# Optimization experiments

Hardware: AMD Instinct MI355X
Metric: run time of the kernel (lower is better)

## Reference

```python
import math
import jax, jax.numpy as jnp
import numpy as np

WS = 4            # window size
LS = 2 * WS       # local context size
NH = 8            # num heads
DIM = 128
EPS = 1e-5


def setup_inputs() -> dict:
    key = jax.random.key(0)
    ks = jax.random.split(key, 8)
    B, C, H, W = 4, DIM, 48, 48
    features = jax.random.normal(ks[0], (B, C, H, W), dtype=jnp.float32)
    s = 0.02
    return {
        'features': features,
        'ln_w': jnp.ones((C,), jnp.float32),
        'ln_b': jnp.zeros((C,), jnp.float32),
        'q_w': jax.random.normal(ks[1], (C, C), jnp.float32) * s,
        'q_b': jnp.zeros((C,), jnp.float32),
        'kv_w': jax.random.normal(ks[2], (2 * C, C), jnp.float32) * s,
        'kv_b': jnp.zeros((2 * C,), jnp.float32),
        'out_w': jax.random.normal(ks[3], (C, C), jnp.float32) * s,
        'out_b': jnp.zeros((C,), jnp.float32),
    }


def _avgpool_tokens(x, k):
    # x: [B,C,H,W] -> [B, (H//k)*(W//k), C]
    B, C, H, W = x.shape
    t = x.reshape(B, C, H // k, k, W // k, k).mean(axis=(3, 5))
    return t.reshape(B, C, -1).transpose(0, 2, 1)


def reference(features, ln_w, ln_b, q_w, q_b, kv_w, kv_b, out_w, out_b):
    B, C, H, W = features.shape
    Hw, Ww = H // WS, W // WS
    nw = Hw * Ww
    hd = C // NH

    # ---- window partition: [B,C,H,W] -> [B*nw, WS*WS, C]
    qt = features.reshape(B, C, Hw, WS, Ww, WS).transpose(0, 2, 4, 3, 5, 1)
    qt = qt.reshape(B * nw, WS * WS, C)

    # ---- LayerNorm(dim)
    mu = qt.mean(-1, keepdims=True)
    var = qt.var(-1, keepdims=True)
    qt = (qt - mu) / jnp.sqrt(var + EPS) * ln_w + ln_b

    # ---- local context: pad to target, unfold kernel=LS stride=WS
    target = (int(math.sqrt(nw)) - 1) * WS + LS
    ph, pw = max(0, target - H), max(0, target - W)
    pad = ((0, 0), (0, 0), (ph // 2, ph - ph // 2), (pw // 2, pw - pw // 2))
    padded = jnp.pad(features, pad)
    # channel order of patches is (C, kh, kw), same as torch unfold
    patches = jax.lax.conv_general_dilated_patches(
        padded, filter_shape=(LS, LS), window_strides=(WS, WS), padding='VALID')
    local = patches.reshape(B, C, LS * LS, nw).transpose(0, 3, 2, 1)
    local = local.reshape(B * nw, LS * LS, C)

    # ---- multi-scale pooled tokens, broadcast to each window
    mid = _avgpool_tokens(features, 2)      # [B, M, C]
    glo = _avgpool_tokens(features, 4)      # [B, G, C]
    mid = jnp.broadcast_to(mid[:, None], (B, nw) + mid.shape[1:]).reshape(B * nw, -1, C)
    glo = jnp.broadcast_to(glo[:, None], (B, nw) + glo.shape[1:]).reshape(B * nw, -1, C)

    kv_tokens = jnp.concatenate([local, mid, glo], axis=1)  # [B*nw, Nkv, C]

    # ---- projections (torch Linear: x @ W.T + b)
    queries = qt @ q_w.T + q_b
    kv = kv_tokens @ kv_w.T + kv_b
    keys, values = kv[..., :C], kv[..., C:]

    # ---- multi-head attention
    Nq, Nkv = queries.shape[1], keys.shape[1]
    q = queries.reshape(-1, Nq, NH, hd)
    k = keys.reshape(-1, Nkv, NH, hd)
    v = values.reshape(-1, Nkv, NH, hd)
    scores = jnp.einsum('bqhd,bkhd->bhqk', q, k) / math.sqrt(hd)
    weights = jax.nn.softmax(scores, axis=-1)
    attended = jnp.einsum('bhqk,bkhd->bqhd', weights, v).reshape(-1, Nq, C)

    out = attended @ out_w.T + out_b

    # ---- window reconstruction -> [B,C,H,W]
    out = out.reshape(B, Hw, Ww, WS, WS, C).transpose(0, 5, 1, 3, 2, 4)
    out = out.reshape(B, C, H, W)
    return out + features
```

## Files before the change

kernel.cpp:

```cpp
#include <hip/hip_runtime.h>


typedef unsigned short u16;
typedef short v8s __attribute__((ext_vector_type(8)));
typedef v8s __attribute__((may_alias)) v8s_am;
typedef short v4s __attribute__((ext_vector_type(4)));
typedef v4s __attribute__((may_alias)) v4s_am;
typedef float v4f __attribute__((ext_vector_type(4)));

#define MFMA_BF16(a, b, c) __builtin_amdgcn_mfma_f32_16x16x32_bf16(a, b, c, 0, 0, 0)

#if __has_builtin(__builtin_amdgcn_mfma_f32_16x16x16bf16_1k)
#define MFMA16(a, b, c) __builtin_amdgcn_mfma_f32_16x16x16bf16_1k(a, b, c, 0, 0, 0)
#else
static __device__ __forceinline__ v4f mfma16_fb(v4s a, v4s b, v4f c) {
    v8s a8 = {a[0], a[1], a[2], a[3], 0, 0, 0, 0};
    v8s b8 = {b[0], b[1], b[2], b[3], 0, 0, 0, 0};
    return MFMA_BF16(a8, b8, c);
}
#define MFMA16(a, b, c) mfma16_fb(a, b, c)
#endif

#if __has_builtin(__builtin_amdgcn_exp2f)
#define EXP2(x) __builtin_amdgcn_exp2f(x)
#else
#define EXP2(x) exp2f(x)
#endif

__device__ __forceinline__ float b2f(u16 u) {
    union { unsigned int i; float f; } x;
    x.i = ((unsigned int)u) << 16;
    return x.f;
}
__device__ __forceinline__ u16 f2b(float f) {
    union { float f; unsigned int i; } x;
    x.f = f;
    unsigned int u = x.i;
    return (u16)((u + 0x7fffu + ((u >> 16) & 1u)) >> 16);
}

__global__ __launch_bounds__(256) void k_prep_gemm(
    const float* __restrict__ F,
    const float* __restrict__ qw, const float* __restrict__ kvw,
    const float* __restrict__ ow,
    const float* __restrict__ lnw, const float* __restrict__ lnb,
    const float* __restrict__ kvb,
    u16* __restrict__ Xt, u16* __restrict__ Wb, float* __restrict__ MuRs,
    u16* __restrict__ KVg, u16* __restrict__ VTg)
{
    __shared__ u16 SH[17408];
    int blk = blockIdx.x;
    int t = threadIdx.x;

    if (blk >= 304) {
        u16 (*Al)[136] = (u16(*)[136])SH;
        u16 (*Wl)[136] = (u16(*)[136])(SH + 8704);
        int gb = blk - 304;
        int tm = (gb % 45) * 64, tn = (gb / 45) * 64;
        {
            int seg = t & 15, r0 = t >> 4;
#pragma unroll
            for (int i = 0; i < 4; ++i) {
                int r = r0 + 16 * i;
                const float* src = kvw + (size_t)(tn + r) * 128 + seg * 8;
                float4 v0 = *(const float4*)src;
                float4 v1 = *(const float4*)(src + 4);
                v8s o = {(short)f2b(v0.x), (short)f2b(v0.y), (short)f2b(v0.z), (short)f2b(v0.w),
                         (short)f2b(v1.x), (short)f2b(v1.y), (short)f2b(v1.z), (short)f2b(v1.w)};
                *(v8s_am*)&Wl[r][seg * 8] = o;
            }
        }
        {
            int rs = t >> 2;
            int cp = (t & 3) * 32;
            int m = tm + rs;
            float s[32];
            if (m < 2304) {
                int bb = m / 576, loc = m % 576;
                int ii = loc / 24, jj2 = loc % 24;
                const float* f0 = F + (size_t)(bb * 128 + cp) * 2304 + (2 * ii) * 48 + 2 * jj2;
#pragma unroll
                for (int cc = 0; cc < 32; ++cc) {
                    const float* src = f0 + (size_t)cc * 2304;
                    float2 a = *(const float2*)src;
                    float2 d = *(const float2*)(src + 48);
                    s[cc] = (a.x + a.y + d.x + d.y) * 0.25f;
                }
            } else {
                int r2 = m - 2304;
                int bb = r2 / 144, loc = r2 % 144;
                int ii = loc / 12, jj2 = loc % 12;
                const float* f0 = F + (size_t)(bb * 128 + cp) * 2304 + (4 * ii) * 48 + 4 * jj2;
#pragma unroll
                for (int cc = 0; cc < 32; ++cc) {
                    const float* src = f0 + (size_t)cc * 2304;
                    float ss = 0.f;
#pragma unroll
                    for (int di = 0; di < 4; ++di) {
                        float4 v = *(const float4*)(src + di * 48);
                        ss += (v.x + v.y) + (v.z + v.w);
                    }
                    s[cc] = ss * 0.0625f;
                }
            }
#pragma unroll
            for (int k = 0; k < 4; ++k) {
                v8s o;
#pragma unroll
                for (int jj = 0; jj < 8; ++jj) o[jj] = (short)f2b(s[k * 8 + jj]);
                *(v8s_am*)&Al[rs][cp + k * 8] = o;
            }
        }
        __syncthreads();
        int lane = t & 63, wave = t >> 6;
        int n15 = lane & 15, quad = lane >> 4;
        int wm = (wave & 1) * 32, wn = (wave >> 1) * 32;
        v4f acc[2][2] = {};
#pragma unroll
        for (int kc = 0; kc < 4; ++kc) {
            v8s a[2], bb[2];
#pragma unroll
            for (int im = 0; im < 2; ++im)
                a[im] = *(const v8s_am*)&Al[wm + im * 16 + n15][kc * 32 + quad * 8];
#pragma unroll
            for (int in = 0; in < 2; ++in)
                bb[in] = *(const v8s_am*)&Wl[wn + in * 16 + n15][kc * 32 + quad * 8];
#pragma unroll
            for (int im = 0; im < 2; ++im)
#pragma unroll
                for (int in = 0; in < 2; ++in)
                    acc[im][in] = MFMA_BF16(a[im], bb[in], acc[im][in]);
        }
        bool vblk = (tn >= 128);
        bool vfast = vblk && (tm < 2304);
        u16* vt = &Al[0][0];
        if (vfast) __syncthreads();
#pragma unroll
        for (int in = 0; in < 2; ++in) {
            int n = tn + wn + in * 16 + n15;
            float bv = kvb[n];
#pragma unroll
            for (int im = 0; im < 2; ++im) {
                int mbase = tm + wm + im * 16 + quad * 4;
#pragma unroll
                for (int r = 0; r < 4; ++r) {
                    int m = mbase + r;
                    u16 h = f2b(acc[im][in][r] + bv);
                    if (!vblk) {
                        KVg[((size_t)m) * 128 + n] = h;
                    } else if (vfast) {
                        vt[(n - tn) * 72 + (wm + im * 16 + quad * 4 + r)] = h;
                    } else {
                        int ch = n - 128;
                        int r2 = m - 2304;
                        int bb2 = r2 / 144, tok = 576 + r2 % 144;
                        VTg[((size_t)(bb2 * 128 + ch)) * 720 + tok] = h;
                    }
                }
            }
        }
        if (vfast) {
            __syncthreads();
            int ch = t >> 2, seg = t & 3;
            int bb2 = tm / 576, tokbase = tm % 576;
            v8s a0 = *(const v8s_am*)&vt[ch * 72 + seg * 16];
            v8s a1 = *(const v8s_am*)&vt[ch * 72 + seg * 16 + 8];
            size_t d = ((size_t)(bb2 * 128 + (tn - 128) + ch)) * 720 + tokbase + seg * 16;
            *(v8s_am*)&VTg[d]     = a0;
            *(v8s_am*)&VTg[d + 8] = a1;
        }
        return;
    }
    if (blk >= 288) {
        int base = (blk - 288) * 4096 + t * 16;
#pragma unroll
        for (int i = 0; i < 4; ++i) {
            int idx = base + i * 4;
            const float* src; int off;
            if (idx < 16384)      { src = qw;  off = idx; }
            else if (idx < 49152) { src = kvw; off = idx - 16384; }
            else                  { src = ow;  off = idx - 49152; }
            float4 v = *(const float4*)(src + off);
            unsigned long long packed =
                (unsigned long long)f2b(v.x) |
                ((unsigned long long)f2b(v.y) << 16) |
                ((unsigned long long)f2b(v.z) << 32) |
                ((unsigned long long)f2b(v.w) << 48);
            *(unsigned long long*)(Wb + idx) = packed;
        }
        if (blk == 288) {
            Wb[65536 + t] = f2b(t < 128 ? lnw[t] : lnb[t - 128]);
        }
        return;
    }
    u16 (*X)[34] = (u16(*)[34])SH;
    int b = blk / 72;
    int p0 = (blk % 72) * 32;
#pragma unroll 4
    for (int i = 0; i < 16; ++i) {
        int c = i * 8 + (t >> 5);
        int pix = t & 31;
        X[c][pix] = f2b(F[((size_t)(b * 128 + c)) * 2304 + p0 + pix]);
    }
    __syncthreads();
    int pix = t >> 3;
    int c0 = (t & 7) * 16;
    size_t row = (size_t)(b * 2304 + p0 + pix) * 128;
    float s = 0.f, s2 = 0.f;
#pragma unroll
    for (int sg = 0; sg < 2; ++sg) {
        v8s raw;
#pragma unroll
        for (int j = 0; j < 8; ++j) {
            u16 u = X[c0 + sg * 8 + j][pix];
            raw[j] = (short)u;
            float v = b2f(u);
            s += v; s2 += v * v;
        }
        *(v8s_am*)&Xt[row + c0 + sg * 8] = raw;
    }
    s += __shfl_xor(s, 1);  s2 += __shfl_xor(s2, 1);
    s += __shfl_xor(s, 2);  s2 += __shfl_xor(s2, 2);
    s += __shfl_xor(s, 4);  s2 += __shfl_xor(s2, 4);
    if ((t & 7) == 0) {
        float mean = s * (1.f / 128.f);
        float var = s2 * (1.f / 128.f) - mean * mean;
        float rstd = rsqrtf(var + 1e-5f);
        MuRs[(b * 2304 + p0 + pix) * 2]     = mean;
        MuRs[(b * 2304 + p0 + pix) * 2 + 1] = rstd;
    }
}

__global__ __launch_bounds__(512, 4) void k_attn_fused(
    const float* __restrict__ F,
    const u16* __restrict__ Xt,
    const float* __restrict__ MuRs,
    const u16* __restrict__ KVg,
    const u16* __restrict__ VTg,
    const u16* __restrict__ Wb,
    const float* __restrict__ qb,
    const float* __restrict__ kvb,
    const float* __restrict__ ob,
    float* __restrict__ Out)
{
    __shared__ u16 KB[2][64][136];
    __shared__ u16 VtW[8][2][16][68];

    const u16* qwb  = Wb;
    const u16* kvwb = Wb + 16384;
    const u16* owb  = Wb + 49152;
    const u16* lnwb = Wb + 65536;
    const u16* lnbb = Wb + 65664;
    u16* Atp = &VtW[0][0][0][0];

    int blk = blockIdx.x;
    int xcd = blk & 7, jj = blk >> 3;
    int b = xcd >> 1;
    int wr = (xcd & 1) * 6 + jj / 6;
    int wcp = jj % 6;

    int t = threadIdx.x;
    int lane = t & 63, wave = t >> 6, n15 = lane & 15, quad = lane >> 4;
    v8s zf8 = {};
    v4f zz4 = {0.f, 0.f, 0.f, 0.f};
    const float QSCALE = 0.25f * 1.44269504f;

    v8s stg[2];
#pragma unroll
    for (int i = 0; i < 2; ++i) {
        int chunk = i * 512 + t;
        stg[i] = *(const v8s_am*)&KVg[((size_t)(b * 576 + (chunk >> 4))) * 128 + (chunk & 15) * 8];
    }

    v4s qf[2];
#pragma unroll
    for (int wi = 0; wi < 2; ++wi) {
        int wc = wcp * 2 + wi;
        int qh = wr * 4 + (n15 >> 2), qw_ = wc * 4 + (n15 & 3);
        int qpix = b * 2304 + qh * 48 + qw_;
        float mu = MuRs[qpix * 2], rstd = MuRs[qpix * 2 + 1];
        v8s xln[4];
#pragma unroll
        for (int kc = 0; kc < 4; ++kc) {
            v8s x  = *(const v8s_am*)&Xt[(size_t)qpix * 128 + kc * 32 + quad * 8];
            v8s lw = *(const v8s_am*)&lnwb[kc * 32 + quad * 8];
            v8s lb = *(const v8s_am*)&lnbb[kc * 32 + quad * 8];
            v8s y;
#pragma unroll
            for (int j = 0; j < 8; ++j)
                y[j] = (short)f2b((b2f((u16)x[j]) - mu) * rstd * b2f((u16)lw[j]) + b2f((u16)lb[j]));
            xln[kc] = y;
        }
        int n0 = wave * 16;
        v4f qacc = zz4;
#pragma unroll
        for (int kc = 0; kc < 4; ++kc) {
            v8s aw = *(const v8s_am*)&qwb[((size_t)(n0 + n15)) * 128 + kc * 32 + quad * 8];
            qacc = MFMA_BF16(aw, xln[kc], qacc);
        }
        v4s q4;
#pragma unroll
        for (int r = 0; r < 4; ++r)
            q4[r] = (short)f2b((qacc[r] + qb[n0 + quad * 4 + r]) * QSCALE);
        qf[wi] = q4;
    }

    v4s kfloc[2][4];
#pragma unroll
    for (int wi = 0; wi < 2; ++wi) {
        int wc = wcp * 2 + wi;
#pragma unroll
        for (int g = 0; g < 4; ++g) {
            int tl = g * 16 + n15;
            int fh = tl >> 3, fw = tl & 7;
            int hh = wr * 4 - 2 + fh, ww = wc * 4 - 2 + fw;
            bool valid = (hh >= 0 && hh < 48 && ww >= 0 && ww < 48);
            size_t arow = (size_t)(b * 2304 + hh * 48 + ww) * 128;
            v8s xb[4];
#pragma unroll
            for (int kc = 0; kc < 4; ++kc) {
                v8s v = zf8;
                if (valid) v = *(const v8s_am*)&Xt[arow + kc * 32 + quad * 8];
                xb[kc] = v;
            }
#pragma unroll
            for (int s = 0; s < 2; ++s) {
                int sbase = s * 128 + wave * 16;
                v4f acc = zz4;
#pragma unroll
                for (int kc = 0; kc < 4; ++kc) {
                    v8s aw = *(const v8s_am*)&kvwb[((size_t)(sbase + n15)) * 128 + kc * 32 + quad * 8];
                    acc = MFMA_BF16(aw, xb[kc], acc);
                }
                if (s == 0) {
                    v4s k4;
#pragma unroll
                    for (int r = 0; r < 4; ++r)
                        k4[r] = (short)f2b(acc[r] + kvb[sbase + quad * 4 + r]);
                    kfloc[wi][g] = k4;
                } else {
#pragma unroll
                    for (int r = 0; r < 4; ++r)
                        VtW[wave][wi][quad * 4 + r][g * 16 + n15] =
                            f2b(acc[r] + kvb[sbase + quad * 4 + r]);
                }
            }
        }
    }

    v4f oacc[2] = {};
    float ls0 = 0.f, ls1 = 0.f;
    const u16* VTb = VTg + (size_t)b * 92160;

    asm volatile("s_waitcnt lgkmcnt(0)" ::: "memory");
#pragma unroll
    for (int wi = 0; wi < 2; ++wi) {
#pragma unroll
        for (int g = 0; g < 4; ++g) {
            v4f St = MFMA16(kfloc[wi][g], qf[wi], zz4);
            float p0 = EXP2(St[0]), p1 = EXP2(St[1]);
            float p2 = EXP2(St[2]), p3 = EXP2(St[3]);
            if (wi == 0) ls0 += (p0 + p1) + (p2 + p3);
            else         ls1 += (p0 + p1) + (p2 + p3);
            v4s pk = {(short)f2b(p0), (short)f2b(p1), (short)f2b(p2), (short)f2b(p3)};
            v4s vf = *(const v4s_am*)&VtW[wave][wi][n15][g * 16 + quad * 4];
            oacc[wi] = MFMA16(vf, pk, oacc[wi]);
        }
    }

#pragma unroll
    for (int i = 0; i < 2; ++i) {
        int chunk = i * 512 + t;
        *(v8s_am*)&KB[1][chunk >> 4][(chunk & 15) * 8] = stg[i];
    }
    __syncthreads();

    for (int tb = 0; tb <= 10; ++tb) {
        v4s vp[4];
        {
            const u16* vrow = VTb + (size_t)(wave * 16 + n15) * 720 + tb * 64 + quad * 4;
#pragma unroll
            for (int g = 0; g < 4; ++g)
                vp[g] = *(const v4s_am*)(vrow + g * 16);
        }
        int nt_ = tb + 1;
        int rowbase = (nt_ < 9) ? (b * 576 + nt_ * 64)
                                : (2304 + b * 144 + nt_ * 64 - 576);
        int nrows = (nt_ == 11) ? 16 : 64;
        bool sv[2];
#pragma unroll
        for (int i = 0; i < 2; ++i) {
            int chunk = i * 512 + t;
            int rr = chunk >> 4;
            sv[i] = rr < nrows;
            if (sv[i])
                stg[i] = *(const v8s_am*)&KVg[((size_t)(rowbase + rr)) * 128 + (chunk & 15) * 8];
        }
        const u16 (*KBc)[136] = KB[1 - (tb & 1)];
#pragma unroll
        for (int g = 0; g < 4; ++g) {
            v4s kf = *(const v4s_am*)&KBc[g * 16 + n15][wave * 16 + quad * 4];
            v4f St0 = MFMA16(kf, qf[0], zz4);
            v4f St1 = MFMA16(kf, qf[1], zz4);
            float a0 = EXP2(St0[0]), a1 = EXP2(St0[1]), a2 = EXP2(St0[2]), a3 = EXP2(St0[3]);
            float b0 = EXP2(St1[0]), b1 = EXP2(St1[1]), b2 = EXP2(St1[2]), b3 = EXP2(St1[3]);
            ls0 += (a0 + a1) + (a2 + a3);
            ls1 += (b0 + b1) + (b2 + b3);
            v4s pk0 = {(short)f2b(a0), (short)f2b(a1), (short)f2b(a2), (short)f2b(a3)};
            v4s pk1 = {(short)f2b(b0), (short)f2b(b1), (short)f2b(b2), (short)f2b(b3)};
            oacc[0] = MFMA16(vp[g], pk0, oacc[0]);
            oacc[1] = MFMA16(vp[g], pk1, oacc[1]);
        }
#pragma unroll
        for (int i = 0; i < 2; ++i) {
            if (sv[i]) {
                int chunk = i * 512 + t;
                *(v8s_am*)&KB[tb & 1][chunk >> 4][(chunk & 15) * 8] = stg[i];
            }
        }
        __syncthreads();
    }
    {
        v4s vf = *(const v4s_am*)(VTb + (size_t)(wave * 16 + n15) * 720 + 704 + quad * 4);
        v4s kf = *(const v4s_am*)&KB[0][n15][wave * 16 + quad * 4];
        v4f St0 = MFMA16(kf, qf[0], zz4);
        v4f St1 = MFMA16(kf, qf[1], zz4);
        float a0 = EXP2(St0[0]), a1 = EXP2(St0[1]), a2 = EXP2(St0[2]), a3 = EXP2(St0[3]);
        float b0 = EXP2(St1[0]), b1 = EXP2(St1[1]), b2 = EXP2(St1[2]), b3 = EXP2(St1[3]);
        ls0 += (a0 + a1) + (a2 + a3);
        ls1 += (b0 + b1) + (b2 + b3);
        v4s pk0 = {(short)f2b(a0), (short)f2b(a1), (short)f2b(a2), (short)f2b(a3)};
        v4s pk1 = {(short)f2b(b0), (short)f2b(b1), (short)f2b(b2), (short)f2b(b3)};
        oacc[0] = MFMA16(vf, pk0, oacc[0]);
        oacc[1] = MFMA16(vf, pk1, oacc[1]);
    }

#pragma unroll
    for (int wi = 0; wi < 2; ++wi) {
        float ls = wi == 0 ? ls0 : ls1;
        ls += __shfl_xor(ls, 16);
        ls += __shfl_xor(ls, 32);
        float inv = 1.f / ls;
        v4s a4 = {(short)f2b(oacc[wi][0] * inv), (short)f2b(oacc[wi][1] * inv),
                  (short)f2b(oacc[wi][2] * inv), (short)f2b(oacc[wi][3] * inv)};
        *(v4s_am*)&Atp[wi * 2176 + n15 * 136 + wave * 16 + quad * 4] = a4;
    }
    __syncthreads();

#pragma unroll
    for (int wi = 0; wi < 2; ++wi) {
        int wc = wcp * 2 + wi;
        int n0 = wave * 16;
        v4f oa = zz4;
#pragma unroll
        for (int kc = 0; kc < 4; ++kc) {
            v8s af = *(const v8s_am*)&Atp[wi * 2176 + n15 * 136 + kc * 32 + quad * 8];
            v8s bf = *(const v8s_am*)&owb[((size_t)(n0 + n15)) * 128 + kc * 32 + quad * 8];
            oa = MFMA_BF16(af, bf, oa);
        }
        int c = n0 + n15;
        float bv = ob[c];
#pragma unroll
        for (int r = 0; r < 4; ++r) {
            int pix = quad * 4 + r;
            int hh = wr * 4 + (pix >> 2), ww_ = wc * 4 + (pix & 3);
            size_t idx = ((size_t)(b * 128 + c)) * 2304 + hh * 48 + ww_;
            Out[idx] = oa[r] + bv + F[idx];
        }
    }
}

extern "C" void kernel_launch(void* const* d_in, const int* in_sizes, int n_in,
                              void* d_out, int out_size, void* d_ws, size_t ws_size,
                              hipStream_t stream)
{
    const float* F   = (const float*)d_in[0];
    const float* lnw = (const float*)d_in[1];
    const float* lnb = (const float*)d_in[2];
    const float* qw  = (const float*)d_in[3];
    const float* qb  = (const float*)d_in[4];
    const float* kvw = (const float*)d_in[5];
    const float* kvb = (const float*)d_in[6];
    const float* ow  = (const float*)d_in[7];
    const float* ob  = (const float*)d_in[8];
    float* Out = (float*)d_out;

    u16* ws    = (u16*)d_ws;
    u16* Xt    = ws;
    u16* Pml   = Xt + 9216 * 128;
    u16* KVg   = Pml + 2880 * 128;
    u16* VTg   = KVg + 2880 * 128;
    u16* Wb    = VTg + 4 * 128 * 720;
    float* MuRs = (float*)(Wb + 65792);

    k_prep_gemm<<<484, 256, 0, stream>>>(F, qw, kvw, ow, lnw, lnb, kvb,
                                         Xt, Wb, MuRs, KVg, VTg);
    k_attn_fused<<<288, 512, 0, stream>>>(F, Xt, MuRs, KVg, VTg, Wb,
                                          qb, kvb, ob, Out);
}
```

Measured before the change: 139.6 us.

## Give each wave private K slices with register prefetch, dropping per-tile block barriers

The shared 64x128 K tile, which every iteration refilled cooperatively behind a __syncthreads, becomes a per-wave 64x16 slice. Each wave loads only its own head's columns and double-buffers them in LDS, so the 11-iteration loop no longer needs block-wide barriers. K and V loads are software-pipelined two tiles ahead in registers. The residual F values are prefetched before the loop to hide their latency at the epilogue. This costs more registers under the 512x4 launch bounds, and the tail-tile index handling is delicate.

```diff
diff --git a/kernel.cpp b/kernel.cpp
--- a/kernel.cpp
+++ b/kernel.cpp
@@ -37,6 +37,10 @@
     x.f = f;
     unsigned int u = x.i;
     return (u16)((u + 0x7fffu + ((u >> 16) & 1u)) >> 16);
+}
+
+__device__ __forceinline__ int rbase_of(int b, int tb) {
+    return (tb < 9) ? (b * 576 + tb * 64) : (2304 + b * 144 + (tb - 9) * 64);
 }
 
 __global__ __launch_bounds__(256) void k_prep_gemm(
@@ -243,7 +247,7 @@
     const float* __restrict__ ob,
     float* __restrict__ Out)
 {
-    __shared__ u16 KB[2][64][136];
+    __shared__ u16 KP[8][2][64][16];
     __shared__ u16 VtW[8][2][16][68];
 
     const u16* qwb  = Wb;
@@ -265,12 +269,19 @@
     v4f zz4 = {0.f, 0.f, 0.f, 0.f};
     const float QSCALE = 0.25f * 1.44269504f;
 
-    v8s stg[2];
-#pragma unroll
-    for (int i = 0; i < 2; ++i) {
-        int chunk = i * 512 + t;
-        stg[i] = *(const v8s_am*)&KVg[((size_t)(b * 576 + (chunk >> 4))) * 128 + (chunk & 15) * 8];
-    }
+    u16* KPw = &KP[wave][0][0][0];
+    const u16* kvcol = KVg + wave * 16;
+    const u16* vrow0 = VTg + (size_t)b * 92160
+                     + (size_t)(wave * 16 + n15) * 720 + quad * 4;
+
+    v8s kC0, kC1;
+    {
+        const u16* s = kvcol + (size_t)(b * 576 + lane) * 128;
+        kC0 = *(const v8s_am*)s; kC1 = *(const v8s_am*)(s + 8);
+    }
+    v4s vpC[4];
+#pragma unroll
+    for (int g = 0; g < 4; ++g) vpC[g] = *(const v4s_am*)(vrow0 + g * 16);
 
     v4s qf[2];
 #pragma unroll
@@ -348,9 +359,20 @@
         }
     }
 
+    *(v8s_am*)&KPw[lane * 16]     = kC0;
+    *(v8s_am*)&KPw[lane * 16 + 8] = kC1;
+
+    v8s kN0, kN1;
+    {
+        const u16* s = kvcol + (size_t)(rbase_of(b, 1) + lane) * 128;
+        kN0 = *(const v8s_am*)s; kN1 = *(const v8s_am*)(s + 8);
+    }
+    v4s vpN[4];
+#pragma unroll
+    for (int g = 0; g < 4; ++g) vpN[g] = *(const v4s_am*)(vrow0 + 64 + g * 16);
+
     v4f oacc[2] = {};
     float ls0 = 0.f, ls1 = 0.f;
-    const u16* VTb = VTg + (size_t)b * 92160;
 
     asm volatile("s_waitcnt lgkmcnt(0)" ::: "memory");
 #pragma unroll
@@ -367,62 +389,70 @@
             oacc[wi] = MFMA16(vf, pk, oacc[wi]);
         }
     }
-
-#pragma unroll
-    for (int i = 0; i < 2; ++i) {
-        int chunk = i * 512 + t;
-        *(v8s_am*)&KB[1][chunk >> 4][(chunk & 15) * 8] = stg[i];
-    }
     __syncthreads();
 
-    for (int tb = 0; tb <= 10; ++tb) {
-        v4s vp[4];
+    float fres[2][4];
+#pragma unroll
+    for (int wi = 0; wi < 2; ++wi) {
+        int wc = wcp * 2 + wi;
+        int c = wave * 16 + n15;
+#pragma unroll
+        for (int r = 0; r < 4; ++r) {
+            int pix = quad * 4 + r;
+            int hh = wr * 4 + (pix >> 2), ww_ = wc * 4 + (pix & 3);
+            fres[wi][r] = F[((size_t)(b * 128 + c)) * 2304 + hh * 48 + ww_];
+        }
+    }
+
+#pragma unroll
+    for (int tb = 0; tb < 11; ++tb) {
+        v8s kX0, kX1; v4s vpX[4];
+        if (tb < 10) {
+            int t2 = tb + 2;
+            int row = (t2 == 11) ? (2304 + b * 144 + 128 + (lane & 15))
+                                 : (rbase_of(b, t2) + lane);
+            const u16* s = kvcol + (size_t)row * 128;
+            kX0 = *(const v8s_am*)s; kX1 = *(const v8s_am*)(s + 8);
+            if (t2 == 11) {
+                vpX[0] = *(const v4s_am*)(vrow0 + 704);
+                vpX[1] = vpX[0]; vpX[2] = vpX[0]; vpX[3] = vpX[0];
+            } else {
+#pragma unroll
+                for (int g = 0; g < 4; ++g)
+                    vpX[g] = *(const v4s_am*)(vrow0 + t2 * 64 + g * 16);
+            }
+        } else { kX0 = kN0; kX1 = kN1; vpX[0] = vpX[1] = vpX[2] = vpX[3] = vpN[0]; }
         {
-            const u16* vrow = VTb + (size_t)(wave * 16 + n15) * 720 + tb * 64 + quad * 4;
-#pragma unroll
-            for (int g = 0; g < 4; ++g)
-                vp[g] = *(const v4s_am*)(vrow + g * 16);
-        }
-        int nt_ = tb + 1;
-        int rowbase = (nt_ < 9) ? (b * 576 + nt_ * 64)
-                                : (2304 + b * 144 + nt_ * 64 - 576);
-        int nrows = (nt_ == 11) ? 16 : 64;
-        bool sv[2];
-#pragma unroll
-        for (int i = 0; i < 2; ++i) {
-            int chunk = i * 512 + t;
-            int rr = chunk >> 4;
-            sv[i] = rr < nrows;
-            if (sv[i])
-                stg[i] = *(const v8s_am*)&KVg[((size_t)(rowbase + rr)) * 128 + (chunk & 15) * 8];
-        }
-        const u16 (*KBc)[136] = KB[1 - (tb & 1)];
-#pragma unroll
-        for (int g = 0; g < 4; ++g) {
-            v4s kf = *(const v4s_am*)&KBc[g * 16 + n15][wave * 16 + quad * 4];
-            v4f St0 = MFMA16(kf, qf[0], zz4);
-            v4f St1 = MFMA16(kf, qf[1], zz4);
-            float a0 = EXP2(St0[0]), a1 = EXP2(St0[1]), a2 = EXP2(St0[2]), a3 = EXP2(St0[3]);
-            float b0 = EXP2(St1[0]), b1 = EXP2(St1[1]), b2 = EXP2(St1[2]), b3 = EXP2(St1[3]);
-            ls0 += (a0 + a1) + (a2 + a3);
-            ls1 += (b0 + b1) + (b2 + b3);
-            v4s pk0 = {(short)f2b(a0), (short)f2b(a1), (short)f2b(a2), (short)f2b(a3)};
-            v4s pk1 = {(short)f2b(b0), (short)f2b(b1), (short)f2b(b2), (short)f2b(b3)};
-            oacc[0] = MFMA16(vp[g], pk0, oacc[0]);
-            oacc[1] = MFMA16(vp[g], pk1, oacc[1]);
-        }
-#pragma unroll
-        for (int i = 0; i < 2; ++i) {
-            if (sv[i]) {
-                int chunk = i * 512 + t;
-                *(v8s_am*)&KB[tb & 1][chunk >> 4][(chunk & 15) * 8] = stg[i];
-            }
-        }
-        __syncthreads();
+            u16* kp1 = KPw + ((tb + 1) & 1) * 1024;
+            *(v8s_am*)&kp1[lane * 16]     = kN0;
+            *(v8s_am*)&kp1[lane * 16 + 8] = kN1;
+        }
+        {
+            const u16* kp0 = KPw + (tb & 1) * 1024;
+#pragma unroll
+            for (int g = 0; g < 4; ++g) {
+                v4s kf = *(const v4s_am*)&kp0[(g * 16 + n15) * 16 + quad * 4];
+                v4f St0 = MFMA16(kf, qf[0], zz4);
+                v4f St1 = MFMA16(kf, qf[1], zz4);
+                float a0 = EXP2(St0[0]), a1 = EXP2(St0[1]), a2 = EXP2(St0[2]), a3 = EXP2(St0[3]);
+                float b0 = EXP2(St1[0]), b1 = EXP2(St1[1]), b2 = EXP2(St1[2]), b3 = EXP2(St1[3]);
+                ls0 += (a0 + a1) + (a2 + a3);
+                ls1 += (b0 + b1) + (b2 + b3);
+                v4s pk0 = {(short)f2b(a0), (short)f2b(a1), (short)f2b(a2), (short)f2b(a3)};
+                v4s pk1 = {(short)f2b(b0), (short)f2b(b1), (short)f2b(b2), (short)f2b(b3)};
+                oacc[0] = MFMA16(vpC[g], pk0, oacc[0]);
+                oacc[1] = MFMA16(vpC[g], pk1, oacc[1]);
+            }
+        }
+#pragma unroll
+        for (int g = 0; g < 4; ++g) vpC[g] = vpN[g];
+        kN0 = kX0; kN1 = kX1;
+#pragma unroll
+        for (int g = 0; g < 4; ++g) vpN[g] = vpX[g];
     }
     {
-        v4s vf = *(const v4s_am*)(VTb + (size_t)(wave * 16 + n15) * 720 + 704 + quad * 4);
-        v4s kf = *(const v4s_am*)&KB[0][n15][wave * 16 + quad * 4];
+        const u16* kp1 = KPw + 1024;
+        v4s kf = *(const v4s_am*)&kp1[n15 * 16 + quad * 4];
         v4f St0 = MFMA16(kf, qf[0], zz4);
         v4f St1 = MFMA16(kf, qf[1], zz4);
         float a0 = EXP2(St0[0]), a1 = EXP2(St0[1]), a2 = EXP2(St0[2]), a3 = EXP2(St0[3]);
@@ -431,8 +461,8 @@
         ls1 += (b0 + b1) + (b2 + b3);
         v4s pk0 = {(short)f2b(a0), (short)f2b(a1), (short)f2b(a2), (short)f2b(a3)};
         v4s pk1 = {(short)f2b(b0), (short)f2b(b1), (short)f2b(b2), (short)f2b(b3)};
-        oacc[0] = MFMA16(vf, pk0, oacc[0]);
-        oacc[1] = MFMA16(vf, pk1, oacc[1]);
+        oacc[0] = MFMA16(vpC[0], pk0, oacc[0]);
+        oacc[1] = MFMA16(vpC[0], pk1, oacc[1]);
     }
 
 #pragma unroll
@@ -465,7 +495,7 @@
             int pix = quad * 4 + r;
             int hh = wr * 4 + (pix >> 2), ww_ = wc * 4 + (pix & 3);
             size_t idx = ((size_t)(b * 128 + c)) * 2304 + hh * 48 + ww_;
-            Out[idx] = oa[r] + bv + F[idx];
+            Out[idx] = oa[r] + bv + fres[wi][r];
         }
     }
 }
```

Measured after the change: 211.0 us. 51.1% more time.
